# Kernel optimization log

Measured on AMD Instinct MI355X. Metric: run time of the kernel, lower is better.

Reference implementation:

```python
import jax, jax.numpy as jnp
import numpy as np

N = 100000   # nodes
E = 1600000  # edges
IN, H, C = 128, 128, 40


def setup_inputs() -> dict:
    key = jax.random.key(0)
    ks = jax.random.split(key, 8)
    feat = jax.random.normal(ks[0], (N, IN), jnp.float32)
    src = jax.random.randint(ks[1], (E,), 0, N, jnp.int32)
    dst = jax.random.randint(ks[2], (E,), 0, N, jnp.int32)
    # Glorot-ish init like dgl GraphConv.reset_parameters
    W0 = jax.random.normal(ks[3], (IN, H), jnp.float32) * (1.0 / np.sqrt(IN))
    W1 = jax.random.normal(ks[4], (H, H), jnp.float32) * (1.0 / np.sqrt(H))
    W2 = jax.random.normal(ks[5], (H, C), jnp.float32) * (1.0 / np.sqrt(H))
    b0 = jnp.zeros((H,), jnp.float32)
    b1 = jnp.zeros((H,), jnp.float32)
    b2 = jnp.zeros((C,), jnp.float32)
    return {"feat": feat, "src": src, "dst": dst,
            "W0": W0, "b0": b0, "W1": W1, "b1": b1, "W2": W2, "b2": b2}


def _graph_conv(h, src, dst, W, b):
    # dgl GraphConv with norm='both': D_out^{-1/2} pre-scale, sum-aggregate,
    # D_in^{-1/2} post-scale; degrees clamped to min 1. Weight applied before
    # aggregation (in_feats >= out_feats path) -- math is identical either way.
    ones = jnp.ones((src.shape[0],), h.dtype)
    deg_out = jnp.maximum(jax.ops.segment_sum(ones, src, num_segments=N), 1.0)
    deg_in = jnp.maximum(jax.ops.segment_sum(ones, dst, num_segments=N), 1.0)
    h = h * (deg_out ** -0.5)[:, None]
    h = h @ W                                   # [N, out]
    agg = jax.ops.segment_sum(h[src], dst, num_segments=N)  # gather+scatter
    return agg * (deg_in ** -0.5)[:, None] + b


def reference(feat, src, dst, W0, b0, W1, b1, W2, b2):
    h = jax.nn.relu(_graph_conv(feat, src, dst, W0, b0))  # dropout p=0 -> identity
    h = jax.nn.relu(_graph_conv(h, src, dst, W1, b1))
    return _graph_conv(h, src, dst, W2, b2)
```

## Files before the change

### kernel.cpp

```cpp
#include <hip/hip_runtime.h>

#define NN 100000
#define EE 1600000
#define ELLW 64
#define NXCD 8
#define RNG ((NN + NXCD - 1) / NXCD)

__device__ __forceinline__ unsigned int pack_bf2(float a, float b) {
    unsigned int ua = __float_as_uint(a);
    ua += 0x7FFFu + ((ua >> 16) & 1u);
    unsigned int ub = __float_as_uint(b);
    ub += 0x7FFFu + ((ub >> 16) & 1u);
    return (ua >> 16) | (ub & 0xFFFF0000u);
}

__global__ __launch_bounds__(256) void k_build(const int* __restrict__ src, const int* __restrict__ dst,
                                               int* __restrict__ din, int* __restrict__ dout,
                                               int* __restrict__ ell, int e) {
    int r = blockIdx.x & (NXCD - 1);
    int slice = blockIdx.x >> 3;
    int i = slice * 256 + threadIdx.x;
    if (i >= e) return;
    int s = __builtin_nontemporal_load(&src[i]);
    int d = __builtin_nontemporal_load(&dst[i]);
    int lo = r * RNG, hi = lo + RNG;
    if (d >= lo && d < hi) {
        int p = atomicAdd(&din[d], 1);
        if (p < ELLW) ell[(size_t)d * ELLW + p] = s;
    }
    if (s >= lo && s < hi) {
        atomicAdd(&dout[s], 1);
    }
}

__global__ __launch_bounds__(256) void k_rsqrt(const int* __restrict__ dout, const int* __restrict__ din,
                                               float* __restrict__ so, float* __restrict__ si, int n) {
    int i = blockIdx.x * 256 + threadIdx.x;
    if (i < n) {
        so[i] = rsqrtf((float)max(1, dout[i]));
        si[i] = rsqrtf((float)max(1, din[i]));
    }
}

__global__ __launch_bounds__(512) void k_gemm128(const float* __restrict__ X, const float* __restrict__ scale,
                                                 const float* __restrict__ W, unsigned int* __restrict__ Y, int n) {
    __shared__ float Xs[128 * 64];
    int tid = threadIdx.x;
    int row0 = blockIdx.x * 64;
    const float4* X4 = (const float4*)X;
    for (int idx = tid; idx < 2048; idx += 512) {
        int r = idx & 63, c4 = idx >> 6;
        int row = row0 + r;
        float4 v = make_float4(0.f, 0.f, 0.f, 0.f);
        float s = 0.f;
        if (row < n) { v = X4[(size_t)row * 32 + c4]; s = scale[row]; }
        Xs[(c4 * 4 + 0) * 64 + r] = v.x * s;
        Xs[(c4 * 4 + 1) * 64 + r] = v.y * s;
        Xs[(c4 * 4 + 2) * 64 + r] = v.z * s;
        Xs[(c4 * 4 + 3) * 64 + r] = v.w * s;
    }
    __syncthreads();
    int cg = tid & 31;
    int rg = tid >> 5;
    float a00=0,a01=0,a02=0,a03=0, a10=0,a11=0,a12=0,a13=0;
    float a20=0,a21=0,a22=0,a23=0, a30=0,a31=0,a32=0,a33=0;
    const float4* W4 = (const float4*)W;
#pragma unroll 4
    for (int k = 0; k < 128; ++k) {
        float4 xv = *(const float4*)&Xs[k * 64 + rg * 4];
        float4 wv = W4[k * 32 + cg];
        a00 += xv.x * wv.x; a01 += xv.x * wv.y; a02 += xv.x * wv.z; a03 += xv.x * wv.w;
        a10 += xv.y * wv.x; a11 += xv.y * wv.y; a12 += xv.y * wv.z; a13 += xv.y * wv.w;
        a20 += xv.z * wv.x; a21 += xv.z * wv.y; a22 += xv.z * wv.z; a23 += xv.z * wv.w;
        a30 += xv.w * wv.x; a31 += xv.w * wv.y; a32 += xv.w * wv.z; a33 += xv.w * wv.w;
    }
    int rbase = row0 + rg * 4;
    uint2* Y2 = (uint2*)Y;
    if (rbase + 0 < n) Y2[(size_t)(rbase + 0) * 32 + cg] = make_uint2(pack_bf2(a00, a01), pack_bf2(a02, a03));
    if (rbase + 1 < n) Y2[(size_t)(rbase + 1) * 32 + cg] = make_uint2(pack_bf2(a10, a11), pack_bf2(a12, a13));
    if (rbase + 2 < n) Y2[(size_t)(rbase + 2) * 32 + cg] = make_uint2(pack_bf2(a20, a21), pack_bf2(a22, a23));
    if (rbase + 3 < n) Y2[(size_t)(rbase + 3) * 32 + cg] = make_uint2(pack_bf2(a30, a31), pack_bf2(a32, a33));
}

__global__ __launch_bounds__(320) void k_gemm40(const float* __restrict__ X, const float* __restrict__ scale,
                                                const float* __restrict__ W, float* __restrict__ Y, int n) {
    __shared__ float Xs[128 * 64];
    int tid = threadIdx.x;
    int row0 = blockIdx.x * 64;
    const float4* X4 = (const float4*)X;
    for (int idx = tid; idx < 2048; idx += 320) {
        int r = idx & 63, c4 = idx >> 6;
        int row = row0 + r;
        float4 v = make_float4(0.f, 0.f, 0.f, 0.f);
        float s = 0.f;
        if (row < n) { v = X4[(size_t)row * 32 + c4]; s = scale[row]; }
        Xs[(c4 * 4 + 0) * 64 + r] = v.x * s;
        Xs[(c4 * 4 + 1) * 64 + r] = v.y * s;
        Xs[(c4 * 4 + 2) * 64 + r] = v.z * s;
        Xs[(c4 * 4 + 3) * 64 + r] = v.w * s;
    }
    __syncthreads();
    int cg = tid % 20;
    int rg = tid / 20;
    float a0x=0,a0y=0, a1x=0,a1y=0, a2x=0,a2y=0, a3x=0,a3y=0;
    const float2* W2 = (const float2*)W;
#pragma unroll 4
    for (int k = 0; k < 128; ++k) {
        float4 xv = *(const float4*)&Xs[k * 64 + rg * 4];
        float2 wv = W2[k * 20 + cg];
        a0x += xv.x * wv.x; a0y += xv.x * wv.y;
        a1x += xv.y * wv.x; a1y += xv.y * wv.y;
        a2x += xv.z * wv.x; a2y += xv.z * wv.y;
        a3x += xv.w * wv.x; a3y += xv.w * wv.y;
    }
    int rbase = row0 + rg * 4;
    float2* Y2 = (float2*)Y;
    if (rbase + 0 < n) Y2[(size_t)(rbase + 0) * 20 + cg] = make_float2(a0x, a0y);
    if (rbase + 1 < n) Y2[(size_t)(rbase + 1) * 20 + cg] = make_float2(a1x, a1y);
    if (rbase + 2 < n) Y2[(size_t)(rbase + 2) * 20 + cg] = make_float2(a2x, a2y);
    if (rbase + 3 < n) Y2[(size_t)(rbase + 3) * 20 + cg] = make_float2(a3x, a3y);
}

__global__ __launch_bounds__(256) void k_gather128(const unsigned int* __restrict__ h, const int* __restrict__ din,
                                                   const int* __restrict__ ell, const float* __restrict__ si,
                                                   const float* __restrict__ b, float* __restrict__ out,
                                                   int n, int do_relu) {
    int wv = threadIdx.x >> 6, lane = threadIdx.x & 63;
    int v = blockIdx.x * 4 + wv;
    if (v >= n) return;
    int cnt = min(din[v], ELLW);
    int cl = ell[(size_t)v * ELLW + lane];
    float sx = 0.f, sy = 0.f;
    for (int j = 0; j < cnt; j += 8) {
        int cc[8]; float mk[8]; unsigned int t[8];
#pragma unroll
        for (int k = 0; k < 8; ++k) {
            int jj = j + k;
            cc[k] = __shfl(cl, jj < cnt ? jj : cnt - 1);
            mk[k] = (jj < cnt) ? 1.f : 0.f;
        }
#pragma unroll
        for (int k = 0; k < 8; ++k)
            t[k] = h[(size_t)cc[k] * 64 + lane];
#pragma unroll
        for (int k = 0; k < 8; ++k) {
            float x = __uint_as_float(t[k] << 16);
            float y = __uint_as_float(t[k] & 0xFFFF0000u);
            sx = fmaf(mk[k], x, sx);
            sy = fmaf(mk[k], y, sy);
        }
    }
    float sc = si[v];
    float2 bb = ((const float2*)b)[lane];
    float ox = sx * sc + bb.x;
    float oy = sy * sc + bb.y;
    if (do_relu) { ox = fmaxf(ox, 0.f); oy = fmaxf(oy, 0.f); }
    ((float2*)out)[(size_t)v * 64 + lane] = make_float2(ox, oy);
}

__global__ __launch_bounds__(256) void k_gather40(const float* __restrict__ h, const int* __restrict__ din,
                                                  const int* __restrict__ ell, const float* __restrict__ si,
                                                  const float* __restrict__ b, float* __restrict__ out, int n) {
    int wv = threadIdx.x >> 6, lane = threadIdx.x & 63;
    int v = blockIdx.x * 4 + wv;
    if (v >= n) return;
    int cnt = min(din[v], ELLW);
    int cl = ell[(size_t)v * ELLW + lane];
    float s = 0.f;
    for (int j = 0; j < cnt; j += 8) {
        int cc[8]; float mk[8]; float t[8];
#pragma unroll
        for (int k = 0; k < 8; ++k) {
            int jj = j + k;
            cc[k] = __shfl(cl, jj < cnt ? jj : cnt - 1);
            mk[k] = (jj < cnt) ? 1.f : 0.f;
        }
        if (lane < 40) {
#pragma unroll
            for (int k = 0; k < 8; ++k) t[k] = h[(size_t)cc[k] * 40 + lane];
#pragma unroll
            for (int k = 0; k < 8; ++k) s = fmaf(mk[k], t[k], s);
        }
    }
    if (lane < 40) {
        out[(size_t)v * 40 + lane] = s * si[v] + b[lane];
    }
}

extern "C" void kernel_launch(void* const* d_in, const int* in_sizes, int n_in,
                              void* d_out, int out_size, void* d_ws, size_t ws_size,
                              hipStream_t stream) {
    const float* feat = (const float*)d_in[0];
    const int*   src  = (const int*)d_in[1];
    const int*   dst  = (const int*)d_in[2];
    const float* W0   = (const float*)d_in[3];
    const float* b0   = (const float*)d_in[4];
    const float* W1   = (const float*)d_in[5];
    const float* b1   = (const float*)d_in[6];
    const float* W2   = (const float*)d_in[7];
    const float* b2   = (const float*)d_in[8];
    float* out = (float*)d_out;

    char* w = (char*)d_ws;
    int*   din       = (int*)w;    w += (size_t)NN * 4;
    int*   dout      = (int*)w;    w += (size_t)NN * 4;
    float* scale_out = (float*)w;  w += (size_t)NN * 4;
    float* scale_in  = (float*)w;  w += (size_t)NN * 4;
    int*   ell       = (int*)w;    w += (size_t)NN * ELLW * 4;
    unsigned int* h2 = (unsigned int*)w; w += (size_t)NN * 128 * 2;
    float* h40       = (float*)w;  w += (size_t)NN * 40 * 4;
    float* agg       = (float*)w;  w += (size_t)NN * 128 * 4;

    hipMemsetAsync(d_ws, 0, (size_t)NN * 8, stream);

    int slices = (EE + 255) / 256;
    k_build<<<slices * NXCD, 256, 0, stream>>>(src, dst, din, dout, ell, EE);
    k_rsqrt<<<(NN + 255) / 256, 256, 0, stream>>>(dout, din, scale_out, scale_in, NN);

    int gemm_grid = (NN + 63) / 64;
    int gath_grid = (NN + 3) / 4;

    k_gemm128<<<gemm_grid, 512, 0, stream>>>(feat, scale_out, W0, h2, NN);
    k_gather128<<<gath_grid, 256, 0, stream>>>(h2, din, ell, scale_in, b0, agg, NN, 1);
    k_gemm128<<<gemm_grid, 512, 0, stream>>>(agg, scale_out, W1, h2, NN);
    k_gather128<<<gath_grid, 256, 0, stream>>>(h2, din, ell, scale_in, b1, agg, NN, 1);
    k_gemm40<<<gemm_grid, 320, 0, stream>>>(agg, scale_out, W2, h40, NN);
    k_gather40<<<gath_grid, 256, 0, stream>>>(h40, din, ell, scale_in, b2, out, NN);
}
```

Baseline: 587.7 us.

## Fuse graph build with first GEMM and fold degree scaling into gathers

The first GEMM now runs unscaled inside the same launch as the ELL/degree build, so the two can overlap. The out-degree normalisation for layer 1 moves into the gather, where each neighbour's weight is rsqrt(dout[src]) shuffled across lanes. The separate rsqrt kernel and its scale arrays are removed; degree scales are recomputed inline from the integer counts. The 128-wide GEMM is retiled to 256 threads with a 4x8 register tile and 128-bit stores. In exchange, layer 1's gather does an extra random dout read per edge, and rounding changes slightly because scaling happens after the bf16 pack.

```diff
diff --git a/kernel.cpp b/kernel.cpp
--- a/kernel.cpp
+++ b/kernel.cpp
@@ -5,6 +5,8 @@
 #define ELLW 64
 #define NXCD 8
 #define RNG ((NN + NXCD - 1) / NXCD)
+#define GEMMN ((NN + 63) / 64)
+#define BUILDN ((EE / 256) * NXCD)
 
 __device__ __forceinline__ unsigned int pack_bf2(float a, float b) {
     unsigned int ua = __float_as_uint(a);
@@ -14,13 +16,74 @@
     return (ua >> 16) | (ub & 0xFFFF0000u);
 }
 
-__global__ __launch_bounds__(256) void k_build(const int* __restrict__ src, const int* __restrict__ dst,
-                                               int* __restrict__ din, int* __restrict__ dout,
-                                               int* __restrict__ ell, int e) {
-    int r = blockIdx.x & (NXCD - 1);
-    int slice = blockIdx.x >> 3;
-    int i = slice * 256 + threadIdx.x;
-    if (i >= e) return;
+__device__ __forceinline__ void gemm128_body(const float* __restrict__ X, const int* __restrict__ dout,
+                                             const float* __restrict__ W, unsigned int* __restrict__ Y,
+                                             int n, int row0, int tid, float* Xs, int scaled) {
+    const float4* X4 = (const float4*)X;
+#pragma unroll
+    for (int idx = tid; idx < 2048; idx += 256) {
+        int r = idx & 63, c4 = idx >> 6;
+        int row = row0 + r;
+        float4 v = make_float4(0.f, 0.f, 0.f, 0.f);
+        float s = 0.f;
+        if (row < n) {
+            v = X4[(size_t)row * 32 + c4];
+            s = scaled ? rsqrtf((float)max(1, dout[row])) : 1.f;
+        }
+        Xs[(c4 * 4 + 0) * 64 + r] = v.x * s;
+        Xs[(c4 * 4 + 1) * 64 + r] = v.y * s;
+        Xs[(c4 * 4 + 2) * 64 + r] = v.z * s;
+        Xs[(c4 * 4 + 3) * 64 + r] = v.w * s;
+    }
+    __syncthreads();
+    int cg = tid & 15;
+    int rg = tid >> 4;
+    float a[4][8];
+#pragma unroll
+    for (int r = 0; r < 4; ++r)
+#pragma unroll
+        for (int c = 0; c < 8; ++c) a[r][c] = 0.f;
+    const float4* W4 = (const float4*)W;
+#pragma unroll 2
+    for (int k = 0; k < 128; ++k) {
+        float4 xv = *(const float4*)&Xs[k * 64 + rg * 4];
+        float4 w0 = W4[k * 32 + cg * 2];
+        float4 w1 = W4[k * 32 + cg * 2 + 1];
+        float xr[4] = {xv.x, xv.y, xv.z, xv.w};
+        float wc[8] = {w0.x, w0.y, w0.z, w0.w, w1.x, w1.y, w1.z, w1.w};
+#pragma unroll
+        for (int r = 0; r < 4; ++r)
+#pragma unroll
+            for (int c = 0; c < 8; ++c) a[r][c] = fmaf(xr[r], wc[c], a[r][c]);
+    }
+    int rbase = row0 + rg * 4;
+    uint4* Y4 = (uint4*)Y;
+#pragma unroll
+    for (int r = 0; r < 4; ++r) {
+        if (rbase + r < n) {
+            Y4[(size_t)(rbase + r) * 16 + cg] =
+                make_uint4(pack_bf2(a[r][0], a[r][1]), pack_bf2(a[r][2], a[r][3]),
+                           pack_bf2(a[r][4], a[r][5]), pack_bf2(a[r][6], a[r][7]));
+        }
+    }
+}
+
+__global__ __launch_bounds__(256) void k_build_gemm0(const int* __restrict__ src, const int* __restrict__ dst,
+                                                     int* __restrict__ din, int* __restrict__ dout,
+                                                     int* __restrict__ ell,
+                                                     const float* __restrict__ X, const float* __restrict__ W,
+                                                     unsigned int* __restrict__ Y) {
+    __shared__ float Xs[128 * 64];
+    int tid = threadIdx.x;
+    if (blockIdx.x < GEMMN) {
+        gemm128_body(X, nullptr, W, Y, NN, blockIdx.x * 64, tid, Xs, 0);
+        return;
+    }
+    int idx = blockIdx.x - GEMMN;
+    int r = idx & (NXCD - 1);
+    int slice = idx >> 3;
+    int i = slice * 256 + tid;
+    if (i >= EE) return;
     int s = __builtin_nontemporal_load(&src[i]);
     int d = __builtin_nontemporal_load(&dst[i]);
     int lo = r * RNG, hi = lo + RNG;
@@ -33,56 +96,13 @@
     }
 }
 
-__global__ __launch_bounds__(256) void k_rsqrt(const int* __restrict__ dout, const int* __restrict__ din,
-                                               float* __restrict__ so, float* __restrict__ si, int n) {
-    int i = blockIdx.x * 256 + threadIdx.x;
-    if (i < n) {
-        so[i] = rsqrtf((float)max(1, dout[i]));
-        si[i] = rsqrtf((float)max(1, din[i]));
-    }
-}
-
-__global__ __launch_bounds__(512) void k_gemm128(const float* __restrict__ X, const float* __restrict__ scale,
+__global__ __launch_bounds__(256) void k_gemm128(const float* __restrict__ X, const int* __restrict__ dout,
                                                  const float* __restrict__ W, unsigned int* __restrict__ Y, int n) {
     __shared__ float Xs[128 * 64];
-    int tid = threadIdx.x;
-    int row0 = blockIdx.x * 64;
-    const float4* X4 = (const float4*)X;
-    for (int idx = tid; idx < 2048; idx += 512) {
-        int r = idx & 63, c4 = idx >> 6;
-        int row = row0 + r;
-        float4 v = make_float4(0.f, 0.f, 0.f, 0.f);
-        float s = 0.f;
-        if (row < n) { v = X4[(size_t)row * 32 + c4]; s = scale[row]; }
-        Xs[(c4 * 4 + 0) * 64 + r] = v.x * s;
-        Xs[(c4 * 4 + 1) * 64 + r] = v.y * s;
-        Xs[(c4 * 4 + 2) * 64 + r] = v.z * s;
-        Xs[(c4 * 4 + 3) * 64 + r] = v.w * s;
-    }
-    __syncthreads();
-    int cg = tid & 31;
-    int rg = tid >> 5;
-    float a00=0,a01=0,a02=0,a03=0, a10=0,a11=0,a12=0,a13=0;
-    float a20=0,a21=0,a22=0,a23=0, a30=0,a31=0,a32=0,a33=0;
-    const float4* W4 = (const float4*)W;
-#pragma unroll 4
-    for (int k = 0; k < 128; ++k) {
-        float4 xv = *(const float4*)&Xs[k * 64 + rg * 4];
-        float4 wv = W4[k * 32 + cg];
-        a00 += xv.x * wv.x; a01 += xv.x * wv.y; a02 += xv.x * wv.z; a03 += xv.x * wv.w;
-        a10 += xv.y * wv.x; a11 += xv.y * wv.y; a12 += xv.y * wv.z; a13 += xv.y * wv.w;
-        a20 += xv.z * wv.x; a21 += xv.z * wv.y; a22 += xv.z * wv.z; a23 += xv.z * wv.w;
-        a30 += xv.w * wv.x; a31 += xv.w * wv.y; a32 += xv.w * wv.z; a33 += xv.w * wv.w;
-    }
-    int rbase = row0 + rg * 4;
-    uint2* Y2 = (uint2*)Y;
-    if (rbase + 0 < n) Y2[(size_t)(rbase + 0) * 32 + cg] = make_uint2(pack_bf2(a00, a01), pack_bf2(a02, a03));
-    if (rbase + 1 < n) Y2[(size_t)(rbase + 1) * 32 + cg] = make_uint2(pack_bf2(a10, a11), pack_bf2(a12, a13));
-    if (rbase + 2 < n) Y2[(size_t)(rbase + 2) * 32 + cg] = make_uint2(pack_bf2(a20, a21), pack_bf2(a22, a23));
-    if (rbase + 3 < n) Y2[(size_t)(rbase + 3) * 32 + cg] = make_uint2(pack_bf2(a30, a31), pack_bf2(a32, a33));
-}
-
-__global__ __launch_bounds__(320) void k_gemm40(const float* __restrict__ X, const float* __restrict__ scale,
+    gemm128_body(X, dout, W, Y, n, blockIdx.x * 64, threadIdx.x, Xs, 1);
+}
+
+__global__ __launch_bounds__(320) void k_gemm40(const float* __restrict__ X, const int* __restrict__ dout,
                                                 const float* __restrict__ W, float* __restrict__ Y, int n) {
     __shared__ float Xs[128 * 64];
     int tid = threadIdx.x;
@@ -93,7 +113,7 @@
         int row = row0 + r;
         float4 v = make_float4(0.f, 0.f, 0.f, 0.f);
         float s = 0.f;
-        if (row < n) { v = X4[(size_t)row * 32 + c4]; s = scale[row]; }
+        if (row < n) { v = X4[(size_t)row * 32 + c4]; s = rsqrtf((float)max(1, dout[row])); }
         Xs[(c4 * 4 + 0) * 64 + r] = v.x * s;
         Xs[(c4 * 4 + 1) * 64 + r] = v.y * s;
         Xs[(c4 * 4 + 2) * 64 + r] = v.z * s;
@@ -122,22 +142,28 @@
 }
 
 __global__ __launch_bounds__(256) void k_gather128(const unsigned int* __restrict__ h, const int* __restrict__ din,
-                                                   const int* __restrict__ ell, const float* __restrict__ si,
+                                                   const int* __restrict__ dout, const int* __restrict__ ell,
                                                    const float* __restrict__ b, float* __restrict__ out,
-                                                   int n, int do_relu) {
+                                                   int n, int do_relu, int so_mode) {
     int wv = threadIdx.x >> 6, lane = threadIdx.x & 63;
     int v = blockIdx.x * 4 + wv;
     if (v >= n) return;
-    int cnt = min(din[v], ELLW);
+    int dv = din[v];
+    int cnt = min(dv, ELLW);
     int cl = ell[(size_t)v * ELLW + lane];
+    int cls = (lane < cnt) ? cl : 0;
+    float scl = 1.f;
+    if (so_mode) scl = rsqrtf((float)max(1, dout[cls]));
     float sx = 0.f, sy = 0.f;
     for (int j = 0; j < cnt; j += 8) {
         int cc[8]; float mk[8]; unsigned int t[8];
 #pragma unroll
         for (int k = 0; k < 8; ++k) {
             int jj = j + k;
-            cc[k] = __shfl(cl, jj < cnt ? jj : cnt - 1);
-            mk[k] = (jj < cnt) ? 1.f : 0.f;
+            int jc = jj < cnt ? jj : cnt - 1;
+            cc[k] = __shfl(cls, jc);
+            float sw = __shfl(scl, jc);
+            mk[k] = (jj < cnt) ? sw : 0.f;
         }
 #pragma unroll
         for (int k = 0; k < 8; ++k)
@@ -150,7 +176,7 @@
             sy = fmaf(mk[k], y, sy);
         }
     }
-    float sc = si[v];
+    float sc = rsqrtf((float)max(1, dv));
     float2 bb = ((const float2*)b)[lane];
     float ox = sx * sc + bb.x;
     float oy = sy * sc + bb.y;
@@ -159,20 +185,22 @@
 }
 
 __global__ __launch_bounds__(256) void k_gather40(const float* __restrict__ h, const int* __restrict__ din,
-                                                  const int* __restrict__ ell, const float* __restrict__ si,
+                                                  const int* __restrict__ ell,
                                                   const float* __restrict__ b, float* __restrict__ out, int n) {
     int wv = threadIdx.x >> 6, lane = threadIdx.x & 63;
     int v = blockIdx.x * 4 + wv;
     if (v >= n) return;
-    int cnt = min(din[v], ELLW);
+    int dv = din[v];
+    int cnt = min(dv, ELLW);
     int cl = ell[(size_t)v * ELLW + lane];
+    int cls = (lane < cnt) ? cl : 0;
     float s = 0.f;
     for (int j = 0; j < cnt; j += 8) {
         int cc[8]; float mk[8]; float t[8];
 #pragma unroll
         for (int k = 0; k < 8; ++k) {
             int jj = j + k;
-            cc[k] = __shfl(cl, jj < cnt ? jj : cnt - 1);
+            cc[k] = __shfl(cls, jj < cnt ? jj : cnt - 1);
             mk[k] = (jj < cnt) ? 1.f : 0.f;
         }
         if (lane < 40) {
@@ -183,7 +211,7 @@
         }
     }
     if (lane < 40) {
-        out[(size_t)v * 40 + lane] = s * si[v] + b[lane];
+        out[(size_t)v * 40 + lane] = s * rsqrtf((float)max(1, dv)) + b[lane];
     }
 }
 
@@ -204,8 +232,6 @@
     char* w = (char*)d_ws;
     int*   din       = (int*)w;    w += (size_t)NN * 4;
     int*   dout      = (int*)w;    w += (size_t)NN * 4;
-    float* scale_out = (float*)w;  w += (size_t)NN * 4;
-    float* scale_in  = (float*)w;  w += (size_t)NN * 4;
     int*   ell       = (int*)w;    w += (size_t)NN * ELLW * 4;
     unsigned int* h2 = (unsigned int*)w; w += (size_t)NN * 128 * 2;
     float* h40       = (float*)w;  w += (size_t)NN * 40 * 4;
@@ -213,17 +239,12 @@
 
     hipMemsetAsync(d_ws, 0, (size_t)NN * 8, stream);
 
-    int slices = (EE + 255) / 256;
-    k_build<<<slices * NXCD, 256, 0, stream>>>(src, dst, din, dout, ell, EE);
-    k_rsqrt<<<(NN + 255) / 256, 256, 0, stream>>>(dout, din, scale_out, scale_in, NN);
-
-    int gemm_grid = (NN + 63) / 64;
     int gath_grid = (NN + 3) / 4;
 
-    k_gemm128<<<gemm_grid, 512, 0, stream>>>(feat, scale_out, W0, h2, NN);
-    k_gather128<<<gath_grid, 256, 0, stream>>>(h2, din, ell, scale_in, b0, agg, NN, 1);
-    k_gemm128<<<gemm_grid, 512, 0, stream>>>(agg, scale_out, W1, h2, NN);
-    k_gather128<<<gath_grid, 256, 0, stream>>>(h2, din, ell, scale_in, b1, agg, NN, 1);
-    k_gemm40<<<gemm_grid, 320, 0, stream>>>(agg, scale_out, W2, h40, NN);
-    k_gather40<<<gath_grid, 256, 0, stream>>>(h40, din, ell, scale_in, b2, out, NN);
-}
+    k_build_gemm0<<<GEMMN + BUILDN, 256, 0, stream>>>(src, dst, din, dout, ell, feat, W0, h2);
+    k_gather128<<<gath_grid, 256, 0, stream>>>(h2, din, dout, ell, b0, agg, NN, 1, 1);
+    k_gemm128<<<GEMMN, 256, 0, stream>>>(agg, dout, W1, h2, NN);
+    k_gather128<<<gath_grid, 256, 0, stream>>>(h2, din, dout, ell, b1, agg, NN, 1, 0);
+    k_gemm40<<<GEMMN, 320, 0, stream>>>(agg, dout, W2, h40, NN);
+    k_gather40<<<gath_grid, 256, 0, stream>>>(h40, din, ell, b2, out, NN);
+}
```

After: 579.9 us. About the same (-1.3%).
